# Optimization experiments

Measured on AMD Instinct MI355X. Metric: run time of the kernel, lower is better.

Reference implementation:

```python
import jax, jax.numpy as jnp
import numpy as np

B, T, DIM, UNITS, OUT = 64, 240, 512, 1024, 75


def setup_inputs() -> dict:
    key = jax.random.key(0)
    keys = iter(jax.random.split(key, 40))

    def w(shape, scale=0.05):
        return jax.random.normal(next(keys), shape, dtype=jnp.float32) * scale

    inp = {
        "in_audio": w((B, T, DIM), 1.0),   # per-step CNN audio features
        "curr_step": w((B, OUT), 1.0),      # initial motion pose
    }

    def add_cell(name, in_dim, u):
        inp[name + "_Wx"] = w((in_dim, 4 * u))
        inp[name + "_Wh"] = w((u, 4 * u))
        inp[name + "_b"] = jnp.zeros((4 * u,), jnp.float32)

    add_cell("enc1", DIM, UNITS)
    add_cell("enc2", UNITS, UNITS)
    add_cell("enc3", UNITS, UNITS)
    inp["fc_W"] = w((UNITS, DIM))
    inp["fc_b"] = jnp.zeros((DIM,), jnp.float32)
    add_cell("dec1", OUT + DIM, UNITS)
    add_cell("dec2", UNITS, UNITS)
    add_cell("dec3", UNITS, UNITS)
    inp["out_W"] = w((UNITS, OUT))
    inp["out_b"] = jnp.zeros((OUT,), jnp.float32)
    return inp


def _lstm(x, h, c, Wx, Wh, b):
    # standard LSTM cell, gate order i, f, g, o
    z = x @ Wx + h @ Wh + b                      # [B, 4U]
    i, f, g, o = jnp.split(z, 4, axis=-1)
    c_new = jax.nn.sigmoid(f) * c + jax.nn.sigmoid(i) * jnp.tanh(g)
    h_new = jax.nn.sigmoid(o) * jnp.tanh(c_new)
    return h_new, c_new


def reference(in_audio, curr_step,
              enc1_Wx, enc1_Wh, enc1_b,
              enc2_Wx, enc2_Wh, enc2_b,
              enc3_Wx, enc3_Wh, enc3_b,
              fc_W, fc_b,
              dec1_Wx, dec1_Wh, dec1_b,
              dec2_Wx, dec2_Wh, dec2_b,
              dec3_Wx, dec3_Wh, dec3_b,
              out_W, out_b):
    Bn = in_audio.shape[0]
    dt = in_audio.dtype
    zu = jnp.zeros((Bn, UNITS), dt)
    carry = (curr_step,
             zu, zu, zu, zu, zu, zu,   # eh1,ec1,eh2,ec2,eh3,ec3
             zu, zu, zu, zu, zu, zu)   # dh1,dc1,dh2,dc2,dh3,dc3

    def step(carry, x):
        (curr, eh1, ec1, eh2, ec2, eh3, ec3,
         dh1, dc1, dh2, dc2, dh3, dc3) = carry
        eh1, ec1 = _lstm(x, eh1, ec1, enc1_Wx, enc1_Wh, enc1_b)
        eh2, ec2 = _lstm(eh1, eh2, ec2, enc2_Wx, enc2_Wh, enc2_b)
        eh3, ec3 = _lstm(eh2, eh3, ec3, enc3_Wx, enc3_Wh, enc3_b)
        _h = jnp.tanh(eh3 @ fc_W + fc_b)          # bottleneck audio code [B, DIM]
        d_in = jnp.concatenate([curr, _h], axis=-1)  # [B, OUT+DIM]
        dh1, dc1 = _lstm(d_in, dh1, dc1, dec1_Wx, dec1_Wh, dec1_b)
        dh2, dc2 = _lstm(dh1, dh2, dc2, dec2_Wx, dec2_Wh, dec2_b)
        dh3, dc3 = _lstm(dh2, dh3, dc3, dec3_Wx, dec3_Wh, dec3_b)
        y = jax.nn.elu(dh3 @ out_W + out_b)       # next motion step [B, OUT]
        new_carry = (y, eh1, ec1, eh2, ec2, eh3, ec3,
                     dh1, dc1, dh2, dc2, dh3, dc3)
        return new_carry, y

    _, ys = jax.lax.scan(step, carry, jnp.swapaxes(in_audio, 0, 1))
    return jnp.swapaxes(ys, 0, 1)  # [B, T, OUT]
```

## Files before the change

kernel.cpp:

```cpp
#include <hip/hip_runtime.h>
#include <hip/hip_bf16.h>
#include <hip/hip_cooperative_groups.h>

namespace cg = cooperative_groups;

typedef __bf16 bf16;
typedef __bf16 bf16x8 __attribute__((ext_vector_type(8)));
typedef float  floatx4 __attribute__((ext_vector_type(4)));
typedef unsigned int uint32;

#define NB   64
#define NT   240
#define NDIM 512
#define NU   1024
#define NOUT 75
#define NWG  64
#define NTHR 1024

#define HSLOT (64 * 1024)
#define YW    80
#define YSLOT (64 * YW)
#define BW    528
#define BSLOT (64 * BW)

struct Params {
  const float* curr;
  const float* bias[8];
  const bf16*  pk[8];
  const bf16*  audio_bf;
  bf16* hr[6];
  bf16* ybuf;
  bf16* hbot;
  uint32* arrv;
  uint32* gof;
  float* out;
  int rmask;
  int pmask;
};

__device__ __forceinline__ float sigmoidf_(float x) { return 1.f / (1.f + __expf(-x)); }

__device__ __forceinline__ void gbar(uint32* arrv, uint32* gof, uint32 sc, int w, int tid)
{
  asm volatile("s_waitcnt vmcnt(0)" ::: "memory");
  __syncthreads();
  if (w == 0) {
    if (tid == 0)
      __hip_atomic_store(&arrv[0], sc, __ATOMIC_RELAXED, __HIP_MEMORY_SCOPE_AGENT);
    if (tid < NWG) {
      int spin = 0;
      while (__hip_atomic_load(&arrv[tid * 32], __ATOMIC_RELAXED, __HIP_MEMORY_SCOPE_AGENT) < sc) {
        __builtin_amdgcn_s_sleep(1);
        if (++spin > (1 << 24)) break;
      }
    }
    __syncthreads();
    if (tid == 0)
      __hip_atomic_store(gof, sc, __ATOMIC_RELAXED, __HIP_MEMORY_SCOPE_AGENT);
  } else {
    if (tid == 0) {
      __hip_atomic_store(&arrv[w * 32], sc, __ATOMIC_RELAXED, __HIP_MEMORY_SCOPE_AGENT);
      int spin = 0;
      while (__hip_atomic_load(gof, __ATOMIC_RELAXED, __HIP_MEMORY_SCOPE_AGENT) < sc) {
        __builtin_amdgcn_s_sleep(1);
        if (++spin > (1 << 24)) break;
      }
    }
    __syncthreads();
  }
}

template<int ST0, int B1, int ST1, int B2, int ST2, int KTOT, int KREAL>
__device__ void lstm_cell(const bf16* __restrict__ p0, const bf16* __restrict__ p1,
                          const bf16* __restrict__ p2,
                          const bf16* __restrict__ pack, const float* __restrict__ bias,
                          bf16* __restrict__ hout, float (* __restrict__ cc)[16],
                          float (* __restrict__ zbuf)[64][16], bf16 (* __restrict__ hstage)[16],
                          char* __restrict__ cb0, char* __restrict__ cb1, char* __restrict__ cb2,
                          int w, int tid)
{
  const int lane = tid & 63, wid = tid >> 6;
  const int g = wid & 3, v = wid >> 2;
  const int lq = lane >> 4, lr = lane & 15;
  constexpr int NCH = KTOT / 128;

  auto issue = [&](int J, char* bufp) {
    #pragma unroll
    for (int ii = 0; ii < 2; ++ii) {
      const int idx = 2 * wid + ii;
      const int kb  = (idx >> 2) & 3;
      const int sel = idx & 3;
      if (idx < 16) {
        int kq = J * 128 + kb * 32 + lq * 8;
        if constexpr (KREAL < KTOT) { if (kq >= KREAL) kq = B2; }
        const int row = 16 * sel + lr;
        const bf16* src;
        if (kq < B1)      src = p0 + (size_t)row * ST0 + kq;
        else if (kq < B2) src = p1 + (size_t)row * ST1 + (kq - B1);
        else              src = p2 + (size_t)row * ST2 + (kq - B2);
        __builtin_amdgcn_global_load_lds((const uint32*)src,
            (uint32*)(bufp + (kb * 4 + sel) * 1024), 16, 0, 0);
      } else {
        const int kq8 = J * 16 + kb * 4 + lq;
        const bf16* src = pack + ((size_t)kq8 * 4096 + 1024 * sel + 16 * w + lr) * 8;
        __builtin_amdgcn_global_load_lds((const uint32*)src,
            (uint32*)(bufp + 16384 + (kb * 4 + sel) * 1024), 16, 0, 0);
      }
    }
  };

  floatx4 c = {0.f, 0.f, 0.f, 0.f};
  auto compute = [&](const char* bufp) {
    #pragma unroll
    for (int kb = 0; kb < 4; ++kb) {
      bf16x8 af  = *(const bf16x8*)(bufp + (kb * 4 + v) * 1024 + lane * 16);
      bf16x8 bfr = *(const bf16x8*)(bufp + 16384 + (kb * 4 + g) * 1024 + lane * 16);
      c = __builtin_amdgcn_mfma_f32_16x16x32_bf16(af, bfr, c, 0, 0, 0);
    }
  };

  char *pA = cb0, *pB = cb1, *pC = cb2;
  issue(0, pA);
  issue(1, pB);
  for (int J = 0; J < NCH - 1; ++J) {
    asm volatile("s_waitcnt vmcnt(2)" ::: "memory");
    __builtin_amdgcn_s_barrier();
    asm volatile("" ::: "memory");
    if (J + 2 < NCH) issue(J + 2, pC);
    compute(pA);
    char* t = pA; pA = pB; pB = pC; pC = t;
  }
  asm volatile("s_waitcnt vmcnt(0)" ::: "memory");
  __builtin_amdgcn_s_barrier();
  asm volatile("" ::: "memory");
  compute(pA);

  #pragma unroll
  for (int r = 0; r < 4; ++r)
    zbuf[g][16 * v + lq * 4 + r][lr] = c[r];
  __syncthreads();
  {
    const int m = tid >> 4, u = tid & 15;
    const int uc = 16 * w + u;
    const float zi = zbuf[0][m][u] + bias[uc];
    const float zf = zbuf[1][m][u] + bias[NU + uc];
    const float zg = zbuf[2][m][u] + bias[2 * NU + uc];
    const float zo = zbuf[3][m][u] + bias[3 * NU + uc];
    const float cold = cc[m][u];
    const float cn = sigmoidf_(zf) * cold + sigmoidf_(zi) * tanhf(zg);
    cc[m][u] = cn;
    hstage[m][u] = (bf16)(sigmoidf_(zo) * tanhf(cn));
  }
  __syncthreads();
  if (tid < 512) {
    const int m = tid >> 3, up = tid & 7;
    const uint32 vv = *(const uint32*)&hstage[m][2 * up];
    __hip_atomic_store((uint32*)(hout + (size_t)m * NU + 16 * w) + up, vv,
                       __ATOMIC_RELAXED, __HIP_MEMORY_SCOPE_AGENT);
  }
}

template<int NEFF>
__device__ void gemm_small(const bf16* __restrict__ a, const bf16* __restrict__ pack,
                           float (* __restrict__ zbuf)[64][16], int w, int tid)
{
  const int lane = tid & 63, wid = tid >> 6;
  const int v = wid & 3, s = wid >> 2;
  const int lr = lane & 15, lq = lane >> 4;
  const int n0 = 16 * w;

  const bf16* wbase = pack + ((size_t)lq * NEFF + (n0 + lr)) * 8;

  bf16x8 wreg[8];
  #pragma unroll
  for (int i = 0; i < 8; ++i)
    wreg[i] = *(const bf16x8*)(wbase + (size_t)(s + 4 * i) * (4 * NEFF * 8));

  floatx4 c = {0.f,0.f,0.f,0.f};
  const bf16* ab = a + (size_t)(16 * v + lr) * NU;

  bf16x8 xa[2];
  xa[0] = *(const bf16x8*)(ab + s * 32 + lq * 8);
  #pragma unroll
  for (int i = 0; i < 8; ++i) {
    const int cur = i & 1, nxt = cur ^ 1;
    if (i + 1 < 8)
      xa[nxt] = *(const bf16x8*)(ab + (s + 4 * (i + 1)) * 32 + lq * 8);
    c = __builtin_amdgcn_mfma_f32_16x16x32_bf16(xa[cur], wreg[i], c, 0, 0, 0);
  }

  #pragma unroll
  for (int r = 0; r < 4; ++r) zbuf[s][16 * v + lq * 4 + r][lr] = c[r];
  __syncthreads();
}

extern "C" __global__ void __launch_bounds__(NTHR)
dancer_main(Params p)
{
  __shared__ __align__(16) char cbuf[3][32768];
  __shared__ float zbuf[4][64][16];
  __shared__ float cst[6][64][16];
  __shared__ bf16  hstage[64][16];
  cg::grid_group grid = cg::this_grid();
  const int tid = threadIdx.x;
  const int w = blockIdx.x;
  const int gtid = w * NTHR + tid;
  const int rmask = p.rmask, pmask = p.pmask;

  if (tid == 0) {
    p.arrv[w * 32] = 0;
    if (w == 0) *p.gof = 0;
  }
  for (int i = gtid; i < 6 * NB * NU; i += NWG * NTHR) {
    const int b = i >> 16, off = i & 65535;
    p.hr[b][(size_t)rmask * HSLOT + off] = (bf16)0.f;
  }
  for (int i = gtid; i < NB * YW; i += NWG * NTHR) {
    const int m = i / YW, c = i - m * YW;
    p.ybuf[i] = (c < NOUT) ? (bf16)p.curr[m * NOUT + c] : (bf16)0.f;
  }
  for (int i = gtid; i < (rmask + 1) * NB * 16; i += NWG * NTHR) {
    const int slot = i >> 10, m = (i >> 4) & 63, cix = i & 15;
    p.hbot[(size_t)slot * BSLOT + (size_t)m * BW + 512 + cix] = (bf16)0.f;
  }
  for (int i = tid; i < 6 * 64 * 16; i += NTHR) (&cst[0][0][0])[i] = 0.f;
  __syncthreads();
  grid.sync();

  uint32 sc = 1;
  for (int t = 0; t < NT; ++t) {
    const int st_ = t & rmask;
    const int sp_ = (t - 1) & rmask;
    __syncthreads();

    lstm_cell<NT * NDIM, NDIM, NU, NDIM, NU, NDIM + NU, NDIM + NU>(
        p.audio_bf + t * NDIM, p.hr[0] + (size_t)sp_ * HSLOT, p.hr[0] + (size_t)sp_ * HSLOT,
        p.pk[0], p.bias[0], p.hr[0] + (size_t)st_ * HSLOT, cst[0], zbuf, &hstage[0],
        cbuf[0], cbuf[1], cbuf[2], w, tid);
    gbar(p.arrv, p.gof, sc++, w, tid);

    lstm_cell<NU, NU, NU, NU, NU, 2 * NU, 2 * NU>(
        p.hr[0] + (size_t)st_ * HSLOT, p.hr[1] + (size_t)sp_ * HSLOT, p.hr[1] + (size_t)sp_ * HSLOT,
        p.pk[1], p.bias[1], p.hr[1] + (size_t)st_ * HSLOT, cst[1], zbuf, &hstage[0],
        cbuf[0], cbuf[1], cbuf[2], w, tid);
    gbar(p.arrv, p.gof, sc++, w, tid);

    lstm_cell<NU, NU, NU, NU, NU, 2 * NU, 2 * NU>(
        p.hr[1] + (size_t)st_ * HSLOT, p.hr[2] + (size_t)sp_ * HSLOT, p.hr[2] + (size_t)sp_ * HSLOT,
        p.pk[2], p.bias[2], p.hr[2] + (size_t)st_ * HSLOT, cst[2], zbuf, &hstage[0],
        cbuf[0], cbuf[1], cbuf[2], w, tid);
    gbar(p.arrv, p.gof, sc++, w, tid);

    if (w < 32) {
      gemm_small<512>(p.hr[2] + (size_t)st_ * HSLOT, p.pk[3], zbuf, w, tid);
      const int m = tid >> 4, u = tid & 15;
      const float z = zbuf[0][m][u] + zbuf[1][m][u] + zbuf[2][m][u] + zbuf[3][m][u]
                      + p.bias[3][16 * w + u];
      hstage[m][u] = (bf16)tanhf(z);
      __syncthreads();
      if (tid < 512) {
        const int m2 = tid >> 3, up = tid & 7;
        const uint32 v = *(const uint32*)&hstage[m2][2 * up];
        __hip_atomic_store((uint32*)(p.hbot + (size_t)st_ * BSLOT + (size_t)m2 * BW + 16 * w) + up,
                           v, __ATOMIC_RELAXED, __HIP_MEMORY_SCOPE_AGENT);
      }
    }
    gbar(p.arrv, p.gof, sc++, w, tid);

    lstm_cell<YW, YW, BW, YW + BW, NU, 1664, YW + BW + NU>(
        p.ybuf + (size_t)st_ * YSLOT, p.hbot + (size_t)st_ * BSLOT, p.hr[3] + (size_t)sp_ * HSLOT,
        p.pk[4], p.bias[4], p.hr[3] + (size_t)st_ * HSLOT, cst[3], zbuf, &hstage[0],
        cbuf[0], cbuf[1], cbuf[2], w, tid);
    gbar(p.arrv, p.gof, sc++, w, tid);

    lstm_cell<NU, NU, NU, NU, NU, 2 * NU, 2 * NU>(
        p.hr[3] + (size_t)st_ * HSLOT, p.hr[4] + (size_t)sp_ * HSLOT, p.hr[4] + (size_t)sp_ * HSLOT,
        p.pk[5], p.bias[5], p.hr[4] + (size_t)st_ * HSLOT, cst[4], zbuf, &hstage[0],
        cbuf[0], cbuf[1], cbuf[2], w, tid);
    gbar(p.arrv, p.gof, sc++, w, tid);

    lstm_cell<NU, NU, NU, NU, NU, 2 * NU, 2 * NU>(
        p.hr[4] + (size_t)st_ * HSLOT, p.hr[5] + (size_t)sp_ * HSLOT, p.hr[5] + (size_t)sp_ * HSLOT,
        p.pk[6], p.bias[6], p.hr[5] + (size_t)st_ * HSLOT, cst[5], zbuf, &hstage[0],
        cbuf[0], cbuf[1], cbuf[2], w, tid);
    gbar(p.arrv, p.gof, sc++, w, tid);

    if (w < 5) {
      gemm_small<80>(p.hr[5] + (size_t)st_ * HSLOT, p.pk[7], zbuf, w, tid);
      const int m = tid >> 4, u = tid & 15;
      const int n = 16 * w + u;
      float y = 0.f;
      if (n < NOUT) {
        const float z = zbuf[0][m][u] + zbuf[1][m][u] + zbuf[2][m][u] + zbuf[3][m][u]
                        + p.bias[7][n];
        y = (z > 0.f) ? z : (__expf(z) - 1.f);
        p.out[(m * NT + t) * NOUT + n] = y;
      }
      hstage[m][u] = (bf16)y;
      __syncthreads();
      if (tid < 512) {
        const int m2 = tid >> 3, up = tid & 7;
        const uint32 v = *(const uint32*)&hstage[m2][2 * up];
        const size_t sn = (size_t)((t + 1) & rmask) * YSLOT;
        __hip_atomic_store((uint32*)(p.ybuf + sn + (size_t)m2 * YW + 16 * w) + up,
                           v, __ATOMIC_RELAXED, __HIP_MEMORY_SCOPE_AGENT);
      }
    }
    if ((t & pmask) == pmask) grid.sync();
  }
}


__global__ void pack_w(const float* __restrict__ Wx, const float* __restrict__ Wh,
                       int Kx, int KhStart, int Keff, int N, int Neff,
                       bf16* __restrict__ dst)
{
  const int idx = blockIdx.x * blockDim.x + threadIdx.x;
  const int nkb = Keff >> 3;
  const int total = nkb * Neff;
  if (idx >= total) return;
  const int kb = idx / Neff;
  const int n  = idx - kb * Neff;
  bf16x8 o;
  #pragma unroll
  for (int j = 0; j < 8; ++j) {
    const int k = kb * 8 + j;
    float v = 0.f;
    if (n < N) {
      if (k < Kx) v = Wx[(size_t)k * N + n];
      else if (k >= KhStart) v = Wh[(size_t)(k - KhStart) * N + n];
    }
    o[j] = (bf16)v;
  }
  *(bf16x8*)(dst + ((size_t)kb * Neff + n) * 8) = o;
}

__global__ void pack_dec1(const float* __restrict__ Wx, const float* __restrict__ Wh,
                          bf16* __restrict__ dst)
{
  const int idx = blockIdx.x * blockDim.x + threadIdx.x;
  const int total = (1664 >> 3) * 4096;
  if (idx >= total) return;
  const int kb = idx >> 12;
  const int n  = idx & 4095;
  bf16x8 o;
  #pragma unroll
  for (int j = 0; j < 8; ++j) {
    const int k = kb * 8 + j;
    float v = 0.f;
    if (k < 75)                    v = Wx[(size_t)k * 4096 + n];
    else if (k >= 80 && k < 592)   v = Wx[(size_t)(k - 5) * 4096 + n];
    else if (k >= 608 && k < 1632) v = Wh[(size_t)(k - 608) * 4096 + n];
    o[j] = (bf16)v;
  }
  *(bf16x8*)(dst + ((size_t)kb * 4096 + n) * 8) = o;
}

__global__ void cvt_bf16(const float* __restrict__ src, bf16* __restrict__ dst, int n)
{
  const int i = blockIdx.x * blockDim.x + threadIdx.x;
  if (i < n) dst[i] = (bf16)src[i];
}

extern "C" void kernel_launch(void* const* d_in, const int* in_sizes, int n_in,
                              void* d_out, int out_size, void* d_ws, size_t ws_size,
                              hipStream_t stream)
{
  (void)in_sizes; (void)n_in; (void)out_size;

  const float* audio = (const float*)d_in[0];
  const float* curr  = (const float*)d_in[1];
  const float* Wp[8][2] = {
    { (const float*)d_in[2],  (const float*)d_in[3]  },
    { (const float*)d_in[5],  (const float*)d_in[6]  },
    { (const float*)d_in[8],  (const float*)d_in[9]  },
    { (const float*)d_in[11], nullptr                },
    { (const float*)d_in[13], (const float*)d_in[14] },
    { (const float*)d_in[16], (const float*)d_in[17] },
    { (const float*)d_in[19], (const float*)d_in[20] },
    { (const float*)d_in[22], nullptr                },
  };
  const float* bias[8] = {
    (const float*)d_in[4],  (const float*)d_in[7],  (const float*)d_in[10],
    (const float*)d_in[12], (const float*)d_in[15], (const float*)d_in[18],
    (const float*)d_in[21], (const float*)d_in[23],
  };

  const int geo[8][5] = {
    { 512,  512,  1536, 4096, 4096 },
    { 1024, 1024, 2048, 4096, 4096 },
    { 1024, 1024, 2048, 4096, 4096 },
    { 1024, 1024, 1024, 512,  512  },
    { 0,    0,    1664, 4096, 4096 },
    { 1024, 1024, 2048, 4096, 4096 },
    { 1024, 1024, 2048, 4096, 4096 },
    { 1024, 1024, 1024, 75,   80   },
  };

  char* ws = (char*)d_ws;
  size_t off = 0;
  auto take = [&](size_t bytes) -> char* {
    char* p = ws + off;
    off = (off + bytes + 255) & ~(size_t)255;
    return p;
  };

  bf16* audio_bf = (bf16*)take((size_t)NB * NT * NDIM * 2);
  bf16* pk[8];
  for (int i = 0; i < 8; ++i) pk[i] = (bf16*)take((size_t)geo[i][2] * geo[i][4] * 2);
  uint32* arrv = (uint32*)take(64 * 32 * sizeof(uint32));
  uint32* gof  = (uint32*)take(256);

  const size_t slot_bytes = (size_t)6 * HSLOT * 2 + (size_t)YSLOT * 2 + (size_t)BSLOT * 2 + 4096;
  int R = 32;
  while (R > 4 && off + (size_t)R * slot_bytes + (1 << 20) > ws_size) R >>= 1;

  bf16* hr[6];
  for (int i = 0; i < 6; ++i) hr[i] = (bf16*)take((size_t)R * HSLOT * 2);
  bf16* ybuf = (bf16*)take((size_t)R * YSLOT * 2);
  bf16* hbot = (bf16*)take((size_t)R * BSLOT * 2);

  {
    const int n = NB * NT * NDIM;
    cvt_bf16<<<(n + 255) / 256, 256, 0, stream>>>(audio, audio_bf, n);
  }
  for (int i = 0; i < 8; ++i) {
    if (i == 4) {
      const int total = (1664 >> 3) * 4096;
      pack_dec1<<<(total + 255) / 256, 256, 0, stream>>>(Wp[4][0], Wp[4][1], pk[4]);
    } else {
      const int total = (geo[i][2] >> 3) * geo[i][4];
      pack_w<<<(total + 255) / 256, 256, 0, stream>>>(
          Wp[i][0], Wp[i][1], geo[i][0], geo[i][1], geo[i][2], geo[i][3], geo[i][4], pk[i]);
    }
  }

  Params P;
  P.curr = curr;
  for (int i = 0; i < 8; ++i) { P.bias[i] = bias[i]; P.pk[i] = pk[i]; }
  P.audio_bf = audio_bf;
  for (int i = 0; i < 6; ++i) P.hr[i] = hr[i];
  P.ybuf = ybuf;
  P.hbot = hbot;
  P.arrv = arrv;
  P.gof = gof;
  P.out = (float*)d_out;
  P.rmask = R - 1;
  P.pmask = (R >> 1) - 1;

  void* args[] = { &P };
  (void)hipLaunchCooperativeKernel(reinterpret_cast<void*>(dancer_main),
                                   dim3(NWG), dim3(NTHR), args, 0, stream);
}
```

Baseline: 24.07 ms.

## Use all-to-all flag barrier, deepen LDS prefetch to four stages, keep cell state in registers

The grid barrier is changed from a two-phase scheme (workgroups report to workgroup 0, which then releases a flag) to a flat scheme where every workgroup publishes its counter and polls all 64 counters directly. This removes one round-trip of global-memory latency from each of the seven barriers per timestep. The LSTM weight/activation streaming gains a fourth LDS buffer, so three chunks are in flight instead of two. Cell state moves from shared memory into per-thread registers. The costs are more polling traffic on the counters, extra LDS use, and more register pressure.

```diff
diff --git a/kernel.cpp b/kernel.cpp
--- a/kernel.cpp
+++ b/kernel.cpp
@@ -40,43 +40,30 @@
 
 __device__ __forceinline__ float sigmoidf_(float x) { return 1.f / (1.f + __expf(-x)); }
 
-__device__ __forceinline__ void gbar(uint32* arrv, uint32* gof, uint32 sc, int w, int tid)
+__device__ __forceinline__ void gbar(uint32* arrv, uint32 sc, int w, int tid)
 {
   asm volatile("s_waitcnt vmcnt(0)" ::: "memory");
   __syncthreads();
-  if (w == 0) {
-    if (tid == 0)
-      __hip_atomic_store(&arrv[0], sc, __ATOMIC_RELAXED, __HIP_MEMORY_SCOPE_AGENT);
-    if (tid < NWG) {
-      int spin = 0;
-      while (__hip_atomic_load(&arrv[tid * 32], __ATOMIC_RELAXED, __HIP_MEMORY_SCOPE_AGENT) < sc) {
-        __builtin_amdgcn_s_sleep(1);
-        if (++spin > (1 << 24)) break;
-      }
-    }
-    __syncthreads();
-    if (tid == 0)
-      __hip_atomic_store(gof, sc, __ATOMIC_RELAXED, __HIP_MEMORY_SCOPE_AGENT);
-  } else {
-    if (tid == 0) {
-      __hip_atomic_store(&arrv[w * 32], sc, __ATOMIC_RELAXED, __HIP_MEMORY_SCOPE_AGENT);
-      int spin = 0;
-      while (__hip_atomic_load(gof, __ATOMIC_RELAXED, __HIP_MEMORY_SCOPE_AGENT) < sc) {
-        __builtin_amdgcn_s_sleep(1);
-        if (++spin > (1 << 24)) break;
-      }
-    }
-    __syncthreads();
-  }
+  if (tid == 0)
+    __hip_atomic_store(&arrv[w * 32], sc, __ATOMIC_RELAXED, __HIP_MEMORY_SCOPE_AGENT);
+  if (tid < NWG) {
+    int spin = 0;
+    while (__hip_atomic_load(&arrv[tid * 32], __ATOMIC_RELAXED, __HIP_MEMORY_SCOPE_AGENT) < sc) {
+      __builtin_amdgcn_s_sleep(1);
+      if (++spin > (1 << 24)) break;
+    }
+  }
+  __syncthreads();
 }
 
 template<int ST0, int B1, int ST1, int B2, int ST2, int KTOT, int KREAL>
 __device__ void lstm_cell(const bf16* __restrict__ p0, const bf16* __restrict__ p1,
                           const bf16* __restrict__ p2,
                           const bf16* __restrict__ pack, const float* __restrict__ bias,
-                          bf16* __restrict__ hout, float (* __restrict__ cc)[16],
+                          bf16* __restrict__ hout, float& ccr,
                           float (* __restrict__ zbuf)[64][16], bf16 (* __restrict__ hstage)[16],
-                          char* __restrict__ cb0, char* __restrict__ cb1, char* __restrict__ cb2,
+                          char* __restrict__ cb0, char* __restrict__ cb1,
+                          char* __restrict__ cb2, char* __restrict__ cb3,
                           int w, int tid)
 {
   const int lane = tid & 63, wid = tid >> 6;
@@ -119,17 +106,28 @@
     }
   };
 
-  char *pA = cb0, *pB = cb1, *pC = cb2;
+  char *pA = cb0, *pB = cb1, *pC = cb2, *pD = cb3;
   issue(0, pA);
   issue(1, pB);
-  for (int J = 0; J < NCH - 1; ++J) {
-    asm volatile("s_waitcnt vmcnt(2)" ::: "memory");
+  issue(2, pC);
+  for (int J = 0; J + 3 < NCH; ++J) {
+    asm volatile("s_waitcnt vmcnt(4)" ::: "memory");
     __builtin_amdgcn_s_barrier();
     asm volatile("" ::: "memory");
-    if (J + 2 < NCH) issue(J + 2, pC);
+    issue(J + 3, pD);
     compute(pA);
-    char* t = pA; pA = pB; pB = pC; pC = t;
-  }
+    char* t = pA; pA = pB; pB = pC; pC = pD; pD = t;
+  }
+  asm volatile("s_waitcnt vmcnt(4)" ::: "memory");
+  __builtin_amdgcn_s_barrier();
+  asm volatile("" ::: "memory");
+  compute(pA);
+  { char* t = pA; pA = pB; pB = pC; pC = pD; pD = t; }
+  asm volatile("s_waitcnt vmcnt(2)" ::: "memory");
+  __builtin_amdgcn_s_barrier();
+  asm volatile("" ::: "memory");
+  compute(pA);
+  { char* t = pA; pA = pB; pB = pC; pC = pD; pD = t; }
   asm volatile("s_waitcnt vmcnt(0)" ::: "memory");
   __builtin_amdgcn_s_barrier();
   asm volatile("" ::: "memory");
@@ -146,9 +144,9 @@
     const float zf = zbuf[1][m][u] + bias[NU + uc];
     const float zg = zbuf[2][m][u] + bias[2 * NU + uc];
     const float zo = zbuf[3][m][u] + bias[3 * NU + uc];
-    const float cold = cc[m][u];
+    const float cold = ccr;
     const float cn = sigmoidf_(zf) * cold + sigmoidf_(zi) * tanhf(zg);
-    cc[m][u] = cn;
+    ccr = cn;
     hstage[m][u] = (bf16)(sigmoidf_(zo) * tanhf(cn));
   }
   __syncthreads();
@@ -197,9 +195,8 @@
 extern "C" __global__ void __launch_bounds__(NTHR)
 dancer_main(Params p)
 {
-  __shared__ __align__(16) char cbuf[3][32768];
+  __shared__ __align__(16) char cbuf[4][32768];
   __shared__ float zbuf[4][64][16];
-  __shared__ float cst[6][64][16];
   __shared__ bf16  hstage[64][16];
   cg::grid_group grid = cg::this_grid();
   const int tid = threadIdx.x;
@@ -207,6 +204,8 @@
   const int gtid = w * NTHR + tid;
   const int rmask = p.rmask, pmask = p.pmask;
 
+  float cc0 = 0.f, cc1 = 0.f, cc2 = 0.f, cc3 = 0.f, cc4 = 0.f, cc5 = 0.f;
+
   if (tid == 0) {
     p.arrv[w * 32] = 0;
     if (w == 0) *p.gof = 0;
@@ -223,7 +222,6 @@
     const int slot = i >> 10, m = (i >> 4) & 63, cix = i & 15;
     p.hbot[(size_t)slot * BSLOT + (size_t)m * BW + 512 + cix] = (bf16)0.f;
   }
-  for (int i = tid; i < 6 * 64 * 16; i += NTHR) (&cst[0][0][0])[i] = 0.f;
   __syncthreads();
   grid.sync();
 
@@ -235,21 +233,21 @@
 
     lstm_cell<NT * NDIM, NDIM, NU, NDIM, NU, NDIM + NU, NDIM + NU>(
         p.audio_bf + t * NDIM, p.hr[0] + (size_t)sp_ * HSLOT, p.hr[0] + (size_t)sp_ * HSLOT,
-        p.pk[0], p.bias[0], p.hr[0] + (size_t)st_ * HSLOT, cst[0], zbuf, &hstage[0],
-        cbuf[0], cbuf[1], cbuf[2], w, tid);
-    gbar(p.arrv, p.gof, sc++, w, tid);
+        p.pk[0], p.bias[0], p.hr[0] + (size_t)st_ * HSLOT, cc0, zbuf, &hstage[0],
+        cbuf[0], cbuf[1], cbuf[2], cbuf[3], w, tid);
+    gbar(p.arrv, sc++, w, tid);
 
     lstm_cell<NU, NU, NU, NU, NU, 2 * NU, 2 * NU>(
         p.hr[0] + (size_t)st_ * HSLOT, p.hr[1] + (size_t)sp_ * HSLOT, p.hr[1] + (size_t)sp_ * HSLOT,
-        p.pk[1], p.bias[1], p.hr[1] + (size_t)st_ * HSLOT, cst[1], zbuf, &hstage[0],
-        cbuf[0], cbuf[1], cbuf[2], w, tid);
-    gbar(p.arrv, p.gof, sc++, w, tid);
+        p.pk[1], p.bias[1], p.hr[1] + (size_t)st_ * HSLOT, cc1, zbuf, &hstage[0],
+        cbuf[0], cbuf[1], cbuf[2], cbuf[3], w, tid);
+    gbar(p.arrv, sc++, w, tid);
 
     lstm_cell<NU, NU, NU, NU, NU, 2 * NU, 2 * NU>(
         p.hr[1] + (size_t)st_ * HSLOT, p.hr[2] + (size_t)sp_ * HSLOT, p.hr[2] + (size_t)sp_ * HSLOT,
-        p.pk[2], p.bias[2], p.hr[2] + (size_t)st_ * HSLOT, cst[2], zbuf, &hstage[0],
-        cbuf[0], cbuf[1], cbuf[2], w, tid);
-    gbar(p.arrv, p.gof, sc++, w, tid);
+        p.pk[2], p.bias[2], p.hr[2] + (size_t)st_ * HSLOT, cc2, zbuf, &hstage[0],
+        cbuf[0], cbuf[1], cbuf[2], cbuf[3], w, tid);
+    gbar(p.arrv, sc++, w, tid);
 
     if (w < 32) {
       gemm_small<512>(p.hr[2] + (size_t)st_ * HSLOT, p.pk[3], zbuf, w, tid);
@@ -265,25 +263,25 @@
                            v, __ATOMIC_RELAXED, __HIP_MEMORY_SCOPE_AGENT);
       }
     }
-    gbar(p.arrv, p.gof, sc++, w, tid);
+    gbar(p.arrv, sc++, w, tid);
 
     lstm_cell<YW, YW, BW, YW + BW, NU, 1664, YW + BW + NU>(
         p.ybuf + (size_t)st_ * YSLOT, p.hbot + (size_t)st_ * BSLOT, p.hr[3] + (size_t)sp_ * HSLOT,
-        p.pk[4], p.bias[4], p.hr[3] + (size_t)st_ * HSLOT, cst[3], zbuf, &hstage[0],
-        cbuf[0], cbuf[1], cbuf[2], w, tid);
-    gbar(p.arrv, p.gof, sc++, w, tid);
+        p.pk[4], p.bias[4], p.hr[3] + (size_t)st_ * HSLOT, cc3, zbuf, &hstage[0],
+        cbuf[0], cbuf[1], cbuf[2], cbuf[3], w, tid);
+    gbar(p.arrv, sc++, w, tid);
 
     lstm_cell<NU, NU, NU, NU, NU, 2 * NU, 2 * NU>(
         p.hr[3] + (size_t)st_ * HSLOT, p.hr[4] + (size_t)sp_ * HSLOT, p.hr[4] + (size_t)sp_ * HSLOT,
-        p.pk[5], p.bias[5], p.hr[4] + (size_t)st_ * HSLOT, cst[4], zbuf, &hstage[0],
-        cbuf[0], cbuf[1], cbuf[2], w, tid);
-    gbar(p.arrv, p.gof, sc++, w, tid);
+        p.pk[5], p.bias[5], p.hr[4] + (size_t)st_ * HSLOT, cc4, zbuf, &hstage[0],
+        cbuf[0], cbuf[1], cbuf[2], cbuf[3], w, tid);
+    gbar(p.arrv, sc++, w, tid);
 
     lstm_cell<NU, NU, NU, NU, NU, 2 * NU, 2 * NU>(
         p.hr[4] + (size_t)st_ * HSLOT, p.hr[5] + (size_t)sp_ * HSLOT, p.hr[5] + (size_t)sp_ * HSLOT,
-        p.pk[6], p.bias[6], p.hr[5] + (size_t)st_ * HSLOT, cst[5], zbuf, &hstage[0],
-        cbuf[0], cbuf[1], cbuf[2], w, tid);
-    gbar(p.arrv, p.gof, sc++, w, tid);
+        p.pk[6], p.bias[6], p.hr[5] + (size_t)st_ * HSLOT, cc5, zbuf, &hstage[0],
+        cbuf[0], cbuf[1], cbuf[2], cbuf[3], w, tid);
+    gbar(p.arrv, sc++, w, tid);
 
     if (w < 5) {
       gemm_small<80>(p.hr[5] + (size_t)st_ * HSLOT, p.pk[7], zbuf, w, tid);
```

New measurement: 27.36 ms. 1.14x slower.
